# Kernel optimization log

Measured on AMD Instinct MI355X. Metric: run time of the kernel, lower is better.

The kernel has to match this reference:

```python
import jax, jax.numpy as jnp
import numpy as np

B, NE, NN, L = 64, 256, 1024, 512
F_IN, HID = 128, 128
VOCAB = 50000
ALPHA = 0.2
NEG = -9.0e15


def _leaky(z):
    return jnp.where(z >= 0, z, ALPHA * z)


def hga_layer(x, adj, W, W2, W3, a, a2, wc, transfer, concat):
    # x: [B, NN, Fin], adj: [B, NE, NN] (hyperedge incidence)
    O = W2.shape[1]
    x4 = x @ W2                      # [B, NN, O]
    if transfer:
        x = x @ W                    # [B, NN, O]
    # node->edge attention: score depends only on node k (query is shared word_context)
    s0 = wc[0] @ a[:O, 0]            # scalar
    e1 = _leaky(x4 @ a[O:, 0] + s0)  # [B, NN]
    e1 = jnp.broadcast_to(e1[:, None, :], adj.shape)          # [B, NE, NN]
    att_edge = jax.nn.softmax(jnp.where(adj > 0, e1, NEG), axis=2)
    edge = att_edge @ x              # [B, NE, O]
    edge4 = edge @ W3                # [B, NE, O]
    # edge->node attention: query = node feat x4[k], key = edge feat edge4[j]
    e2 = _leaky((x4 @ a2[:O, 0])[:, None, :] + (edge4 @ a2[O:, 0])[:, :, None])  # [B, NE, NN]
    att_node = jax.nn.softmax(jnp.where(adj > 0, e2, NEG).transpose(0, 2, 1), axis=2)  # [B, NN, NE]
    node = att_node @ edge           # [B, NN, O]
    return jax.nn.elu(node) if concat else node


def setup_inputs() -> dict:
    key = jax.random.key(0)
    ks = jax.random.split(key, 16)
    stdv = 1.0 / np.sqrt(HID)
    u = lambda k, shape: jax.random.uniform(k, shape, jnp.float32, -stdv, stdv)
    inp = {
        "items": jax.random.randint(ks[0], (B, NN), 0, VOCAB),
        "alias_inputs": jax.random.randint(ks[1], (B, L), 0, NN),
        "node_masks": jnp.ones((B, L), jnp.float32),
        "adj": jax.random.randint(ks[2], (B, NE, NN), 0, 2).astype(jnp.float32),
        "emb": jax.random.normal(ks[3], (VOCAB, F_IN), jnp.float32),
        # layer 1 (transfer=False, concat=True)
        "w2_1": u(ks[4], (F_IN, HID)),
        "w3_1": u(ks[5], (HID, HID)),
        "a_1": u(ks[6], (2 * HID, 1)),
        "a2_1": u(ks[7], (2 * HID, 1)),
        "wc_1": u(ks[8], (1, HID)),
        # layer 2 (transfer=True, concat=False)
        "w_2": u(ks[9], (HID, HID)),
        "w2_2": u(ks[10], (HID, HID)),
        "w3_2": u(ks[11], (HID, HID)),
        "a_2": u(ks[12], (2 * HID, 1)),
        "a2_2": u(ks[13], (2 * HID, 1)),
        "wc_2": u(ks[14], (1, HID)),
        "ln_g": jnp.ones((HID,), jnp.float32),
        "ln_b": jnp.zeros((HID,), jnp.float32),
    }
    return inp


def reference(items, alias_inputs, node_masks, adj, emb,
              w2_1, w3_1, a_1, a2_1, wc_1,
              w_2, w2_2, w3_2, a_2, a2_2, wc_2,
              ln_g, ln_b):
    hidden = emb[items]                                        # [B, NN, F]
    x = hga_layer(hidden, adj, None, w2_1, w3_1, a_1, a2_1, wc_1,
                  transfer=False, concat=True)
    x = hga_layer(x, adj, w_2, w2_2, w3_2, a_2, a2_2, wc_2,
                  transfer=True, concat=False)                 # [B, NN, HID]
    seq = jnp.take_along_axis(x, alias_inputs[:, :, None], axis=1)  # [B, L, HID]
    m = node_masks[:, :, None]
    h = seq * m
    b = jnp.sum(h * m, axis=-2) / jnp.sum(node_masks, -1, keepdims=True)  # [B, HID]
    mu = jnp.mean(b, -1, keepdims=True)
    var = jnp.mean((b - mu) ** 2, -1, keepdims=True)
    return (b - mu) / jnp.sqrt(var + 1e-6) * ln_g + ln_b
```

## Files before the change

### kernel.cpp

```cpp
#include <hip/hip_runtime.h>
#include <hip/hip_bf16.h>

typedef __hip_bfloat16 bf16;
typedef __attribute__((ext_vector_type(8))) unsigned short u16x8;
typedef __attribute__((ext_vector_type(4))) unsigned short u16x4;
typedef __attribute__((ext_vector_type(4))) float f32x4;
typedef __attribute__((ext_vector_type(8))) short bf16x8;

#define B_   64
#define NE_  256
#define NN_  1024
#define L_   512
#define HID_ 128
#define ALPHA_ 0.2f

__device__ __forceinline__ float bfu(unsigned short u){
  unsigned int x = ((unsigned int)u) << 16;
  union { unsigned int i; float f; } c; c.i = x; return c.f;
}
__device__ __forceinline__ unsigned short f2b(float f){
  bf16 h = __float2bfloat16(f);
  union { bf16 b; unsigned short u; } c; c.b = h; return c.u;
}
__device__ __forceinline__ int swz(int r, int c){ return (c ^ (r & 3) ^ ((r >> 2) & 3)) & 3; }

__global__ void k_small(const float* __restrict__ w2_1, const float* __restrict__ w3_1,
                        const float* __restrict__ a_1,  const float* __restrict__ a2_1,
                        const float* __restrict__ wc_1,
                        const float* __restrict__ w2_2, const float* __restrict__ w3_2,
                        const float* __restrict__ a_2,  const float* __restrict__ a2_2,
                        const float* __restrict__ wc_2,
                        const float* __restrict__ w_2,
                        const int* __restrict__ alias, const float* __restrict__ masks,
                        float* __restrict__ consts, unsigned short* __restrict__ W2T,
                        float* __restrict__ wcount, float* __restrict__ msum,
                        float* __restrict__ pooled)
{
  __shared__ float wcs[1024];
  __shared__ float red4[4];
  int blk = blockIdx.x, t = threadIdx.x;
  if (blk < 6) {
    if (t < 128) {
      const float* M; const float* v;
      switch (blk) {
        case 0: M = w2_1; v = a_1  + 128; break;
        case 1: M = w2_1; v = a2_1;       break;
        case 2: M = w3_1; v = a2_1 + 128; break;
        case 3: M = w2_2; v = a_2  + 128; break;
        case 4: M = w2_2; v = a2_2;       break;
        default: M = w3_2; v = a2_2 + 128; break;
      }
      float acc = 0.f;
      #pragma unroll 4
      for (int o = 0; o < 128; o += 4) {
        f32x4 m = *(const f32x4*)(M + t*128 + o);
        f32x4 x = *(const f32x4*)(v + o);
        acc += m[0]*x[0] + m[1]*x[1] + m[2]*x[2] + m[3]*x[3];
      }
      consts[blk*128 + t] = acc;
    }
  } else if (blk < 8) {
    const float* wc = (blk == 6) ? wc_1 : wc_2;
    const float* a  = (blk == 6) ? a_1  : a_2;
    if (t < 64) {
      float s = wc[t]*a[t] + wc[t+64]*a[t+64];
      #pragma unroll
      for (int sh = 32; sh > 0; sh >>= 1) s += __shfl_xor(s, sh);
      if (t == 0) consts[768 + (blk - 6)] = s;
    }
  } else if (blk == 8) {
    if (t < 128) for (int k = 0; k < 128; ++k) W2T[t*128 + k] = f2b(w_2[k*128 + t]);
  } else if (blk == 9) {
    for (int i = t; i < B_*HID_; i += 256) pooled[i] = 0.f;
  } else {
    int b = blk - 10;
    #pragma unroll
    for (int j = 0; j < 4; ++j) wcs[t + j*256] = 0.f;
    __syncthreads();
    float s = 0.f;
    #pragma unroll
    for (int j = 0; j < 2; ++j) {
      int l = t + j*256;
      float m = masks[b*L_ + l];
      int idx = alias[b*L_ + l];
      atomicAdd(&wcs[idx], m*m);
      s += m;
    }
    #pragma unroll
    for (int sh = 32; sh > 0; sh >>= 1) s += __shfl_xor(s, sh);
    if ((t & 63) == 0) red4[t >> 6] = s;
    __syncthreads();
    if (t == 0) msum[b] = red4[0] + red4[1] + red4[2] + red4[3];
    #pragma unroll
    for (int j = 0; j < 4; ++j) wcount[(long)b*NN_ + t + j*256] = wcs[t + j*256];
  }
}

__global__ __launch_bounds__(256) void k_prep(
    const float* __restrict__ adj,
    unsigned long long* __restrict__ ADJBb,
    unsigned short* __restrict__ ADJT16)
{
  __shared__ unsigned long long Lbits[16][17];
  const int id = blockIdx.x;
  const int b  = id & 63;
  const int ec = id >> 6;
  const int t  = threadIdx.x;
  const int wv = t >> 6, lane = t & 63;
  const int grp = lane >> 4;
  const int gl  = lane & 15;

  #pragma unroll
  for (int rr = 0; rr < 4; ++rr) {
    const int r = wv*4 + rr;
    const int e = ec*16 + r;
    const float* src = adj + ((long)b*NE_ + e)*NN_;
    #pragma unroll
    for (int i = 0; i < 4; ++i) {
      f32x4 v = *(const f32x4*)(src + i*256 + lane*4);
      unsigned long long nib =
            (unsigned long long)(v[0] != 0.f)
          | ((unsigned long long)(v[1] != 0.f) << 1)
          | ((unsigned long long)(v[2] != 0.f) << 2)
          | ((unsigned long long)(v[3] != 0.f) << 3);
      unsigned long long word = nib << (gl * 4);
      #pragma unroll
      for (int s = 1; s < 16; s <<= 1)
        word |= __shfl_xor(word, s);
      if (gl == 0) {
        Lbits[r][i*4 + grp] = word;
        ADJBb[((long)b*NE_ + e)*16 + i*4 + grp] = word;
      }
    }
  }
  __syncthreads();
  #pragma unroll
  for (int j = 0; j < 4; ++j) {
    int n = t + 256*j;
    int w = n >> 6, bitn = n & 63;
    unsigned int o = 0;
    #pragma unroll
    for (int rr = 0; rr < 16; ++rr)
      o |= (unsigned int)((Lbits[rr][w] >> bitn) & 1ull) << rr;
    ADJT16[((long)b*NN_ + n)*16 + ec] = (unsigned short)o;
  }
}

__global__ void k_fproj(const float* __restrict__ emb, const int* __restrict__ gitems,
                        const float* __restrict__ consts,
                        float* __restrict__ w1, float* __restrict__ f1,
                        unsigned short* __restrict__ YT)
{
  __shared__ float ce1s[128], cf1s[128];
  __shared__ __attribute__((aligned(16))) unsigned short T[64][132];
  int b = blockIdx.y, n0 = blockIdx.x * 64, t = threadIdx.x;
  if (t < 128) { ce1s[t] = consts[t]; cf1s[t] = consts[128 + t]; }
  __syncthreads();
  int r = t >> 2, h0 = (t & 3) * 32;
  long row = (long)b*NN_ + n0 + r;
  float s0 = consts[768];
  float xv[32];
  const float* sp = emb + (long)gitems[row]*HID_ + h0;
  #pragma unroll
  for (int j = 0; j < 32; j += 4) {
    f32x4 v = *(const f32x4*)(sp + j);
    #pragma unroll
    for (int k = 0; k < 4; ++k) xv[j+k] = v[k];
  }
  float p1 = 0.f, p2 = 0.f;
  #pragma unroll
  for (int j = 0; j < 32; ++j) { p1 += xv[j]*ce1s[h0+j]; p2 += xv[j]*cf1s[h0+j]; }
  p1 += __shfl_xor(p1, 1, 4); p1 += __shfl_xor(p1, 2, 4);
  p2 += __shfl_xor(p2, 1, 4); p2 += __shfl_xor(p2, 2, 4);
  float z = p1 + s0; z = (z >= 0.f) ? z : ALPHA_*z;
  float w = __expf(z);
  if ((t & 3) == 0) { w1[row] = w; f1[row] = p2; }
  #pragma unroll
  for (int j = 0; j < 32; j += 4) {
    u16x4 o;
    #pragma unroll
    for (int k = 0; k < 4; ++k) o[k] = f2b(w * xv[j+k]);
    *(u16x4*)&T[r][h0+j] = o;
  }
  __syncthreads();
  int h = t >> 1, nh = (t & 1) * 32;
  unsigned short* dst = YT + ((long)b*HID_ + h)*NN_ + n0 + nh;
  #pragma unroll
  for (int j = 0; j < 32; j += 8) {
    u16x8 o;
    #pragma unroll
    for (int k = 0; k < 8; ++k) o[k] = T[nh+j+k][h];
    *(u16x8*)&dst[j] = o;
  }
}

template<int TRANSFER>
__global__ __launch_bounds__(256) void k_gemm_edge(
    const unsigned char* __restrict__ ADJ8,
    const unsigned short* __restrict__ YT,
    const float* __restrict__ w1v,
    const float* __restrict__ consts, int layer,
    const unsigned short* __restrict__ W2T,
    unsigned short* __restrict__ ET,
    float* __restrict__ f2o)
{
  __shared__ __attribute__((aligned(16))) unsigned short SM[12288];
  __shared__ float dsum[64];
  const int id = blockIdx.x;
  const int b = id & 63;
  const long e0 = (long)(id >> 6) * 64;
  const int t = threadIdx.x;
  const int lane = t & 63;
  const int w = t >> 6, wm = w >> 1, wn = w & 1;
  const int r4 = t >> 2, c4 = t & 3;
  const int lr = lane & 15, g = lane >> 4;

  f32x4 acc[2][4];
  #pragma unroll
  for (int i = 0; i < 2; ++i)
    #pragma unroll
    for (int j = 0; j < 4; ++j) acc[i][j] = (f32x4){0.f,0.f,0.f,0.f};

  const unsigned char*  Ab = ADJ8 + ((long)b*NE_ + e0 + r4)*(NN_ >> 3);
  const unsigned short* Bb = YT + (long)b*HID_*NN_;
  const float*          wb = w1v + (long)b*NN_;

  unsigned int ab; u16x8 bv0, bv1; f32x4 wv0, wv1;
  float dot = 0.f;

  auto stage = [&](int kc) {
    ab  = Ab[(kc >> 3) + c4];
    wv0 = *(const f32x4*)(wb + kc + c4*8);
    wv1 = *(const f32x4*)(wb + kc + c4*8 + 4);
    bv0 = *(const u16x8*)(Bb + (long)r4*NN_ + kc + c4*8);
    bv1 = *(const u16x8*)(Bb + (long)(64+r4)*NN_ + kc + c4*8);
  };
  auto commit = [&](int buf) {
    u16x8 av;
    #pragma unroll
    for (int j = 0; j < 8; ++j) {
      unsigned int bit = (ab >> j) & 1u;
      av[j] = bit ? (unsigned short)0x3F80 : (unsigned short)0;
      float wj = (j < 4) ? wv0[j] : wv1[j-4];
      dot += bit ? wj : 0.f;
    }
    *(u16x8*)&SM[buf*2048 + r4*32 + swz(r4,c4)*8] = av;
    *(u16x8*)&SM[4096 + buf*4096 + r4*32 + swz(r4,c4)*8] = bv0;
    *(u16x8*)&SM[4096 + buf*4096 + (64+r4)*32 + swz(64+r4,c4)*8] = bv1;
  };

  stage(0); commit(0);
  int cur = 0;
  const int NIT = NN_/32;
  for (int it = 0; it < NIT; ++it) {
    __syncthreads();
    if (it+1 < NIT) stage((it+1)*32);
    const unsigned short* AsB = &SM[cur*2048];
    const unsigned short* BsB = &SM[4096 + cur*4096];
    bf16x8 af[2], bfr[4];
    #pragma unroll
    for (int mt = 0; mt < 2; ++mt) {
      int r = wm*32 + mt*16 + lr;
      af[mt] = *(const bf16x8*)&AsB[r*32 + swz(r,g)*8];
    }
    #pragma unroll
    for (int nt = 0; nt < 4; ++nt) {
      int n = wn*64 + nt*16 + lr;
      bfr[nt] = *(const bf16x8*)&BsB[n*32 + swz(n,g)*8];
    }
    #pragma unroll
    for (int mt = 0; mt < 2; ++mt)
      #pragma unroll
      for (int nt = 0; nt < 4; ++nt)
        acc[mt][nt] = __builtin_amdgcn_mfma_f32_16x16x32_bf16(af[mt], bfr[nt], acc[mt][nt], 0, 0, 0);
    if (it+1 < NIT) { commit(cur^1); cur ^= 1; }
  }
  dot += __shfl_down(dot, 2, 4); dot += __shfl_down(dot, 1, 4);
  if ((lane & 3) == 0) dsum[r4] = dot;
  __syncthreads();
  #pragma unroll
  for (int mt = 0; mt < 2; ++mt)
    #pragma unroll
    for (int nt = 0; nt < 4; ++nt) {
      int col = wn*64 + nt*16 + lr;
      #pragma unroll
      for (int q = 0; q < 4; ++q) {
        int rl = wm*32 + mt*16 + g*4 + q;
        SM[rl*136 + col] = f2b(acc[mt][nt][q] / dsum[rl]);
      }
    }
  __syncthreads();
  if (TRANSFER) {
    f32x4 acc2[2][4];
    #pragma unroll
    for (int i = 0; i < 2; ++i)
      #pragma unroll
      for (int j = 0; j < 4; ++j) acc2[i][j] = (f32x4){0.f,0.f,0.f,0.f};
    #pragma unroll
    for (int kc2 = 0; kc2 < 4; ++kc2) {
      bf16x8 af[2], bfr[4];
      #pragma unroll
      for (int mt = 0; mt < 2; ++mt) {
        int r = wm*32 + mt*16 + lr;
        af[mt] = *(const bf16x8*)&SM[r*136 + kc2*32 + g*8];
      }
      #pragma unroll
      for (int nt = 0; nt < 4; ++nt) {
        int n = wn*64 + nt*16 + lr;
        bfr[nt] = *(const bf16x8*)(W2T + n*128 + kc2*32 + g*8);
      }
      #pragma unroll
      for (int mt = 0; mt < 2; ++mt)
        #pragma unroll
        for (int nt = 0; nt < 4; ++nt)
          acc2[mt][nt] = __builtin_amdgcn_mfma_f32_16x16x32_bf16(af[mt], bfr[nt], acc2[mt][nt], 0, 0, 0);
    }
    __syncthreads();
    #pragma unroll
    for (int mt = 0; mt < 2; ++mt)
      #pragma unroll
      for (int nt = 0; nt < 4; ++nt) {
        int col = wn*64 + nt*16 + lr;
        #pragma unroll
        for (int q = 0; q < 4; ++q) {
          int rl = wm*32 + mt*16 + g*4 + q;
          SM[rl*136 + col] = f2b(acc2[mt][nt][q]);
        }
      }
    __syncthreads();
  }
  {
    const float* cf2 = consts + layer*384 + 256;
    int r = t >> 2, h0 = (t & 3) * 32;
    float p = 0.f;
    #pragma unroll
    for (int j = 0; j < 32; ++j) p += bfu(SM[r*136 + h0 + j]) * cf2[h0 + j];
    p += __shfl_down(p, 2, 4); p += __shfl_down(p, 1, 4);
    if ((t & 3) == 0) f2o[(long)b*NE_ + e0 + r] = p;
  }
  {
    int h = t >> 1, eh = (t & 1) * 32;
    unsigned short* dst = ET + ((long)b*HID_ + h)*NE_ + e0 + eh;
    #pragma unroll
    for (int j = 0; j < 32; j += 8) {
      u16x8 o;
      #pragma unroll
      for (int k = 0; k < 8; ++k) o[k] = SM[(eh+j+k)*136 + h];
      *(u16x8*)&dst[j] = o;
    }
  }
}

template<int EPI>
__global__ __launch_bounds__(256, 2) void k_gemm_att(
    const unsigned char* __restrict__ ADJ8,
    const unsigned short* __restrict__ ET,
    const float* __restrict__ f1v, const float* __restrict__ f2v,
    const float* __restrict__ consts,
    unsigned short* __restrict__ YTout, float* __restrict__ w1o, float* __restrict__ f1o,
    const float* __restrict__ wcount, float* __restrict__ pooled)
{
  __shared__ __attribute__((aligned(16))) unsigned short SM[12288];
  __shared__ float dsum[64];
  __shared__ float colsum[128];
  __shared__ float wrow[64];
  const int id = blockIdx.x;
  const int b = id & 63;
  const long m0 = (long)(id >> 6) * 64;
  const int t = threadIdx.x;
  const int lane = t & 63;
  const int w = t >> 6, wm = w >> 1, wn = w & 1;
  const int r4 = t >> 2, c4 = t & 3;
  const int lr = lane & 15, g = lane >> 4;

  f32x4 acc[2][4];
  #pragma unroll
  for (int i = 0; i < 2; ++i)
    #pragma unroll
    for (int j = 0; j < 4; ++j) acc[i][j] = (f32x4){0.f,0.f,0.f,0.f};

  const float f1r = f1v[(long)b*NN_ + m0 + r4];
  const unsigned char*  Ab = ADJ8 + ((long)b*NN_ + m0 + r4)*(NE_ >> 3);
  const unsigned short* Bb = ET + (long)b*HID_*NE_;
  const float* f2p = f2v + (long)b*NE_;

  unsigned int ab; u16x8 bv0, bv1; f32x4 fv0, fv1;
  float dot = 0.f;

  auto stage = [&](int kc) {
    ab  = Ab[(kc >> 3) + c4];
    fv0 = *(const f32x4*)(f2p + kc + c4*8);
    fv1 = *(const f32x4*)(f2p + kc + c4*8 + 4);
    bv0 = *(const u16x8*)(Bb + (long)r4*NE_ + kc + c4*8);
    bv1 = *(const u16x8*)(Bb + (long)(64+r4)*NE_ + kc + c4*8);
  };
  auto commit = [&](int buf) {
    u16x8 av;
    #pragma unroll
    for (int j = 0; j < 8; ++j) {
      unsigned int bit = (ab >> j) & 1u;
      float z = f1r + ((j < 4) ? fv0[j] : fv1[j-4]);
      z = (z >= 0.f) ? z : ALPHA_ * z;
      float wt = bit ? __expf(z) : 0.f;
      unsigned short us = f2b(wt);
      av[j] = us; dot += bfu(us);
    }
    *(u16x8*)&SM[buf*2048 + r4*32 + swz(r4,c4)*8] = av;
    *(u16x8*)&SM[4096 + buf*4096 + r4*32 + swz(r4,c4)*8] = bv0;
    *(u16x8*)&SM[4096 + buf*4096 + (64+r4)*32 + swz(64+r4,c4)*8] = bv1;
  };

  stage(0); commit(0);
  int cur = 0;
  const int NIT = NE_/32;
  for (int it = 0; it < NIT; ++it) {
    __syncthreads();
    if (it+1 < NIT) stage((it+1)*32);
    const unsigned short* AsB = &SM[cur*2048];
    const unsigned short* BsB = &SM[4096 + cur*4096];
    bf16x8 af[2], bfr[4];
    #pragma unroll
    for (int mt = 0; mt < 2; ++mt) {
      int r = wm*32 + mt*16 + lr;
      af[mt] = *(const bf16x8*)&AsB[r*32 + swz(r,g)*8];
    }
    #pragma unroll
    for (int nt = 0; nt < 4; ++nt) {
      int n = wn*64 + nt*16 + lr;
      bfr[nt] = *(const bf16x8*)&BsB[n*32 + swz(n,g)*8];
    }
    #pragma unroll
    for (int mt = 0; mt < 2; ++mt)
      #pragma unroll
      for (int nt = 0; nt < 4; ++nt)
        acc[mt][nt] = __builtin_amdgcn_mfma_f32_16x16x32_bf16(af[mt], bfr[nt], acc[mt][nt], 0, 0, 0);
    if (it+1 < NIT) { commit(cur^1); cur ^= 1; }
  }
  dot += __shfl_down(dot, 2, 4); dot += __shfl_down(dot, 1, 4);
  if ((lane & 3) == 0) dsum[r4] = dot;
  if (EPI == 2 && t < 128) colsum[t] = 0.f;
  __syncthreads();

  if (EPI == 1) {
    #pragma unroll
    for (int mt = 0; mt < 2; ++mt)
      #pragma unroll
      for (int nt = 0; nt < 4; ++nt) {
        int col = wn*64 + nt*16 + lr;
        #pragma unroll
        for (int q = 0; q < 4; ++q) {
          int rl = wm*32 + mt*16 + g*4 + q;
          float v = acc[mt][nt][q] / dsum[rl];
          v = (v > 0.f) ? v : expm1f(v);
          SM[rl*136 + col] = f2b(v);
        }
      }
    __syncthreads();
    {
      const float* ce1 = consts + 384;
      const float* cf1 = consts + 512;
      int r = t >> 2, h0 = (t & 3) * 32;
      float p1 = 0.f, p2 = 0.f;
      #pragma unroll
      for (int j = 0; j < 32; ++j) {
        float xv = bfu(SM[r*136 + h0 + j]);
        p1 += xv * ce1[h0 + j];
        p2 += xv * cf1[h0 + j];
      }
      p1 += __shfl_down(p1, 2, 4); p1 += __shfl_down(p1, 1, 4);
      p2 += __shfl_down(p2, 2, 4); p2 += __shfl_down(p2, 1, 4);
      if ((t & 3) == 0) {
        float z = p1 + consts[769];
        z = (z >= 0.f) ? z : ALPHA_ * z;
        float wv = __expf(z);
        wrow[r] = wv;
        w1o[(long)b*NN_ + m0 + r] = wv;
        f1o[(long)b*NN_ + m0 + r] = p2;
      }
    }
    __syncthreads();
    {
      int h = t >> 1, nh = (t & 1) * 32;
      unsigned short* dst = YTout + ((long)b*HID_ + h)*NN_ + m0 + nh;
      #pragma unroll
      for (int j = 0; j < 32; j += 8) {
        u16x8 o;
        #pragma unroll
        for (int k = 0; k < 8; ++k) {
          int rr = nh + j + k;
          o[k] = f2b(wrow[rr] * bfu(SM[rr*136 + h]));
        }
        *(u16x8*)&dst[j] = o;
      }
    }
  } else {
    float psum[4] = {0.f, 0.f, 0.f, 0.f};
    #pragma unroll
    for (int mt = 0; mt < 2; ++mt)
      #pragma unroll
      for (int q = 0; q < 4; ++q) {
        int rl = wm*32 + mt*16 + g*4 + q;
        float wc = wcount[(long)b*NN_ + m0 + rl];
        float inv = wc / dsum[rl];
        #pragma unroll
        for (int nt = 0; nt < 4; ++nt) psum[nt] += inv * acc[mt][nt][q];
      }
    #pragma unroll
    for (int nt = 0; nt < 4; ++nt) atomicAdd(&colsum[wn*64 + nt*16 + lr], psum[nt]);
    __syncthreads();
    if (t < 128) atomicAdd(&pooled[(long)b*HID_ + t], colsum[t]);
  }
}

__global__ void k_ln(const float* __restrict__ pooled, const float* __restrict__ msum,
                     const float* __restrict__ ln_g, const float* __restrict__ ln_b,
                     float* __restrict__ out)
{
  int b = blockIdx.x, t = threadIdx.x;
  __shared__ float sr[2];
  float bv = pooled[b*HID_ + t] / msum[b];
  int lane = t & 63;
  float p = bv;
  #pragma unroll
  for (int s = 32; s > 0; s >>= 1) p += __shfl_xor(p, s);
  if (lane == 0) sr[t >> 6] = p;
  __syncthreads();
  float mu = (sr[0] + sr[1]) * (1.f / HID_);
  float dv = bv - mu;
  p = dv * dv;
  #pragma unroll
  for (int s = 32; s > 0; s >>= 1) p += __shfl_xor(p, s);
  __syncthreads();
  if (lane == 0) sr[t >> 6] = p;
  __syncthreads();
  float var = (sr[0] + sr[1]) * (1.f / HID_);
  out[b*HID_ + t] = dv / sqrtf(var + 1e-6f) * ln_g[t] + ln_b[t];
}

extern "C" void kernel_launch(void* const* d_in, const int* in_sizes, int n_in,
                              void* d_out, int out_size, void* d_ws, size_t ws_size,
                              hipStream_t stream)
{
  const int*   items = (const int*)d_in[0];
  const int*   alias = (const int*)d_in[1];
  const float* masks = (const float*)d_in[2];
  const float* adj   = (const float*)d_in[3];
  const float* emb   = (const float*)d_in[4];
  const float* w2_1  = (const float*)d_in[5];
  const float* w3_1  = (const float*)d_in[6];
  const float* a_1   = (const float*)d_in[7];
  const float* a2_1  = (const float*)d_in[8];
  const float* wc_1  = (const float*)d_in[9];
  const float* w_2   = (const float*)d_in[10];
  const float* w2_2  = (const float*)d_in[11];
  const float* w3_2  = (const float*)d_in[12];
  const float* a_2   = (const float*)d_in[13];
  const float* a2_2  = (const float*)d_in[14];
  const float* wc_2  = (const float*)d_in[15];
  const float* ln_g  = (const float*)d_in[16];
  const float* ln_b  = (const float*)d_in[17];
  float* out = (float*)d_out;

  char* ws = (char*)d_ws;
  size_t off = 0;
  auto alloc = [&](size_t bytes) -> void* {
    void* p = ws + off; off += (bytes + 255) / 256 * 256; return p;
  };
  unsigned long long* ADJBb = (unsigned long long*)alloc((size_t)B_*NE_*(NN_/8));
  unsigned short*     ADJT16= (unsigned short*)    alloc((size_t)B_*NN_*(NE_/8));
  unsigned short* YT   = (unsigned short*)alloc((size_t)B_*HID_*NN_*2);
  unsigned short* ET   = (unsigned short*)alloc((size_t)B_*HID_*NE_*2);
  float* wcount= (float*)alloc((size_t)B_*NN_*4);
  float* pooled= (float*)alloc((size_t)B_*HID_*4);
  float* w1L1  = (float*)alloc((size_t)B_*NN_*4);
  float* f1L1  = (float*)alloc((size_t)B_*NN_*4);
  float* w1L2  = (float*)alloc((size_t)B_*NN_*4);
  float* f1L2  = (float*)alloc((size_t)B_*NN_*4);
  float* f2    = (float*)alloc((size_t)B_*NE_*4);
  float* msum  = (float*)alloc(B_*4);
  float* consts= (float*)alloc(772*4);
  unsigned short* W2T = (unsigned short*)alloc((size_t)HID_*HID_*2);
  if (off > ws_size) return;

  k_small<<<74, 256, 0, stream>>>(w2_1, w3_1, a_1, a2_1, wc_1, w2_2, w3_2, a_2, a2_2, wc_2,
                                  w_2, alias, masks, consts, W2T, wcount, msum, pooled);
  k_prep<<<B_*16, 256, 0, stream>>>(adj, ADJBb, ADJT16);
  k_fproj<<<dim3(NN_/64, B_), 256, 0, stream>>>(emb, items, consts, w1L1, f1L1, YT);

  k_gemm_edge<0><<<B_*(NE_/64), 256, 0, stream>>>((const unsigned char*)ADJBb, YT, w1L1,
        consts, 0, W2T, ET, f2);
  k_gemm_att<1><<<B_*(NN_/64), 256, 0, stream>>>((const unsigned char*)ADJT16, ET, f1L1, f2,
        consts, YT, w1L2, f1L2, nullptr, nullptr);

  k_gemm_edge<1><<<B_*(NE_/64), 256, 0, stream>>>((const unsigned char*)ADJBb, YT, w1L2,
        consts, 1, W2T, ET, f2);
  k_gemm_att<2><<<B_*(NN_/64), 256, 0, stream>>>((const unsigned char*)ADJT16, ET, f1L2, f2,
        consts, nullptr, nullptr, nullptr, wcount, pooled);

  k_ln<<<B_, HID_, 0, stream>>>(pooled, msum, ln_g, ln_b, out);
}
```

Measured before the change: 129.4 us.

## Retile edge GEMM to 32-row blocks and attention GEMM to 128-row blocks

```diff
diff --git a/kernel.cpp b/kernel.cpp
--- a/kernel.cpp
+++ b/kernel.cpp
@@ -195,7 +195,7 @@
 }
 
 template<int TRANSFER>
-__global__ __launch_bounds__(256) void k_gemm_edge(
+__global__ __launch_bounds__(256, 2) void k_gemm_edge(
     const unsigned char* __restrict__ ADJ8,
     const unsigned short* __restrict__ YT,
     const float* __restrict__ w1v,
@@ -204,49 +204,53 @@
     unsigned short* __restrict__ ET,
     float* __restrict__ f2o)
 {
-  __shared__ __attribute__((aligned(16))) unsigned short SM[12288];
-  __shared__ float dsum[64];
+  __shared__ __attribute__((aligned(16))) unsigned short SM[10240];
+  __shared__ float dsum[32];
   const int id = blockIdx.x;
   const int b = id & 63;
-  const long e0 = (long)(id >> 6) * 64;
+  const long e0 = (long)(id >> 6) * 32;
   const int t = threadIdx.x;
   const int lane = t & 63;
-  const int w = t >> 6, wm = w >> 1, wn = w & 1;
+  const int w = t >> 6;
   const int r4 = t >> 2, c4 = t & 3;
   const int lr = lane & 15, g = lane >> 4;
 
-  f32x4 acc[2][4];
+  f32x4 acc[2][2];
   #pragma unroll
   for (int i = 0; i < 2; ++i)
     #pragma unroll
-    for (int j = 0; j < 4; ++j) acc[i][j] = (f32x4){0.f,0.f,0.f,0.f};
-
-  const unsigned char*  Ab = ADJ8 + ((long)b*NE_ + e0 + r4)*(NN_ >> 3);
+    for (int j = 0; j < 2; ++j) acc[i][j] = (f32x4){0.f,0.f,0.f,0.f};
+
+  const unsigned char*  Ab = ADJ8 + ((long)b*NE_ + e0 + (t < 128 ? r4 : 0))*(NN_ >> 3);
   const unsigned short* Bb = YT + (long)b*HID_*NN_;
   const float*          wb = w1v + (long)b*NN_;
 
-  unsigned int ab; u16x8 bv0, bv1; f32x4 wv0, wv1;
+  unsigned int ab = 0; u16x8 bv0, bv1; f32x4 wv0, wv1;
   float dot = 0.f;
 
   auto stage = [&](int kc) {
-    ab  = Ab[(kc >> 3) + c4];
-    wv0 = *(const f32x4*)(wb + kc + c4*8);
-    wv1 = *(const f32x4*)(wb + kc + c4*8 + 4);
+    if (t < 128) {
+      ab  = Ab[(kc >> 3) + c4];
+      wv0 = *(const f32x4*)(wb + kc + c4*8);
+      wv1 = *(const f32x4*)(wb + kc + c4*8 + 4);
+    }
     bv0 = *(const u16x8*)(Bb + (long)r4*NN_ + kc + c4*8);
     bv1 = *(const u16x8*)(Bb + (long)(64+r4)*NN_ + kc + c4*8);
   };
   auto commit = [&](int buf) {
-    u16x8 av;
-    #pragma unroll
-    for (int j = 0; j < 8; ++j) {
-      unsigned int bit = (ab >> j) & 1u;
-      av[j] = bit ? (unsigned short)0x3F80 : (unsigned short)0;
-      float wj = (j < 4) ? wv0[j] : wv1[j-4];
-      dot += bit ? wj : 0.f;
-    }
-    *(u16x8*)&SM[buf*2048 + r4*32 + swz(r4,c4)*8] = av;
-    *(u16x8*)&SM[4096 + buf*4096 + r4*32 + swz(r4,c4)*8] = bv0;
-    *(u16x8*)&SM[4096 + buf*4096 + (64+r4)*32 + swz(64+r4,c4)*8] = bv1;
+    if (t < 128) {
+      u16x8 av;
+      #pragma unroll
+      for (int j = 0; j < 8; ++j) {
+        unsigned int bit = (ab >> j) & 1u;
+        av[j] = bit ? (unsigned short)0x3F80 : (unsigned short)0;
+        float wj = (j < 4) ? wv0[j] : wv1[j-4];
+        dot += bit ? wj : 0.f;
+      }
+      *(u16x8*)&SM[buf*1024 + r4*32 + swz(r4,c4)*8] = av;
+    }
+    *(u16x8*)&SM[2048 + buf*4096 + r4*32 + swz(r4,c4)*8] = bv0;
+    *(u16x8*)&SM[2048 + buf*4096 + (64+r4)*32 + swz(64+r4,c4)*8] = bv1;
   };
 
   stage(0); commit(0);
@@ -255,75 +259,77 @@
   for (int it = 0; it < NIT; ++it) {
     __syncthreads();
     if (it+1 < NIT) stage((it+1)*32);
-    const unsigned short* AsB = &SM[cur*2048];
-    const unsigned short* BsB = &SM[4096 + cur*4096];
-    bf16x8 af[2], bfr[4];
+    const unsigned short* AsB = &SM[cur*1024];
+    const unsigned short* BsB = &SM[2048 + cur*4096];
+    bf16x8 af[2], bfr[2];
     #pragma unroll
     for (int mt = 0; mt < 2; ++mt) {
-      int r = wm*32 + mt*16 + lr;
+      int r = mt*16 + lr;
       af[mt] = *(const bf16x8*)&AsB[r*32 + swz(r,g)*8];
     }
     #pragma unroll
-    for (int nt = 0; nt < 4; ++nt) {
-      int n = wn*64 + nt*16 + lr;
+    for (int nt = 0; nt < 2; ++nt) {
+      int n = w*32 + nt*16 + lr;
       bfr[nt] = *(const bf16x8*)&BsB[n*32 + swz(n,g)*8];
     }
     #pragma unroll
     for (int mt = 0; mt < 2; ++mt)
       #pragma unroll
-      for (int nt = 0; nt < 4; ++nt)
+      for (int nt = 0; nt < 2; ++nt)
         acc[mt][nt] = __builtin_amdgcn_mfma_f32_16x16x32_bf16(af[mt], bfr[nt], acc[mt][nt], 0, 0, 0);
     if (it+1 < NIT) { commit(cur^1); cur ^= 1; }
   }
-  dot += __shfl_down(dot, 2, 4); dot += __shfl_down(dot, 1, 4);
-  if ((lane & 3) == 0) dsum[r4] = dot;
+  if (t < 128) {
+    dot += __shfl_down(dot, 2, 4); dot += __shfl_down(dot, 1, 4);
+    if ((t & 3) == 0) dsum[r4] = dot;
+  }
   __syncthreads();
   #pragma unroll
   for (int mt = 0; mt < 2; ++mt)
     #pragma unroll
-    for (int nt = 0; nt < 4; ++nt) {
-      int col = wn*64 + nt*16 + lr;
+    for (int nt = 0; nt < 2; ++nt) {
+      int col = w*32 + nt*16 + lr;
       #pragma unroll
       for (int q = 0; q < 4; ++q) {
-        int rl = wm*32 + mt*16 + g*4 + q;
+        int rl = mt*16 + g*4 + q;
         SM[rl*136 + col] = f2b(acc[mt][nt][q] / dsum[rl]);
       }
     }
   __syncthreads();
   if (TRANSFER) {
-    f32x4 acc2[2][4];
+    f32x4 acc2[2][2];
     #pragma unroll
     for (int i = 0; i < 2; ++i)
       #pragma unroll
-      for (int j = 0; j < 4; ++j) acc2[i][j] = (f32x4){0.f,0.f,0.f,0.f};
+      for (int j = 0; j < 2; ++j) acc2[i][j] = (f32x4){0.f,0.f,0.f,0.f};
     #pragma unroll
     for (int kc2 = 0; kc2 < 4; ++kc2) {
-      bf16x8 af[2], bfr[4];
+      bf16x8 af[2], bfr[2];
       #pragma unroll
       for (int mt = 0; mt < 2; ++mt) {
-        int r = wm*32 + mt*16 + lr;
+        int r = mt*16 + lr;
         af[mt] = *(const bf16x8*)&SM[r*136 + kc2*32 + g*8];
       }
       #pragma unroll
-      for (int nt = 0; nt < 4; ++nt) {
-        int n = wn*64 + nt*16 + lr;
+      for (int nt = 0; nt < 2; ++nt) {
+        int n = w*32 + nt*16 + lr;
         bfr[nt] = *(const bf16x8*)(W2T + n*128 + kc2*32 + g*8);
       }
       #pragma unroll
       for (int mt = 0; mt < 2; ++mt)
         #pragma unroll
-        for (int nt = 0; nt < 4; ++nt)
+        for (int nt = 0; nt < 2; ++nt)
           acc2[mt][nt] = __builtin_amdgcn_mfma_f32_16x16x32_bf16(af[mt], bfr[nt], acc2[mt][nt], 0, 0, 0);
     }
     __syncthreads();
     #pragma unroll
     for (int mt = 0; mt < 2; ++mt)
       #pragma unroll
-      for (int nt = 0; nt < 4; ++nt) {
-        int col = wn*64 + nt*16 + lr;
+      for (int nt = 0; nt < 2; ++nt) {
+        int col = w*32 + nt*16 + lr;
         #pragma unroll
         for (int q = 0; q < 4; ++q) {
-          int rl = wm*32 + mt*16 + g*4 + q;
+          int rl = mt*16 + g*4 + q;
           SM[rl*136 + col] = f2b(acc2[mt][nt][q]);
         }
       }
@@ -331,18 +337,18 @@
   }
   {
     const float* cf2 = consts + layer*384 + 256;
-    int r = t >> 2, h0 = (t & 3) * 32;
+    int r = t >> 3, h0 = (t & 7) * 16;
     float p = 0.f;
     #pragma unroll
-    for (int j = 0; j < 32; ++j) p += bfu(SM[r*136 + h0 + j]) * cf2[h0 + j];
-    p += __shfl_down(p, 2, 4); p += __shfl_down(p, 1, 4);
-    if ((t & 3) == 0) f2o[(long)b*NE_ + e0 + r] = p;
+    for (int j = 0; j < 16; ++j) p += bfu(SM[r*136 + h0 + j]) * cf2[h0 + j];
+    p += __shfl_down(p, 4, 8); p += __shfl_down(p, 2, 8); p += __shfl_down(p, 1, 8);
+    if ((t & 7) == 0) f2o[(long)b*NE_ + e0 + r] = p;
   }
   {
-    int h = t >> 1, eh = (t & 1) * 32;
+    int h = t >> 1, eh = (t & 1) * 16;
     unsigned short* dst = ET + ((long)b*HID_ + h)*NE_ + e0 + eh;
     #pragma unroll
-    for (int j = 0; j < 32; j += 8) {
+    for (int j = 0; j < 16; j += 8) {
       u16x8 o;
       #pragma unroll
       for (int k = 0; k < 8; ++k) o[k] = SM[(eh+j+k)*136 + h];
@@ -360,54 +366,61 @@
     unsigned short* __restrict__ YTout, float* __restrict__ w1o, float* __restrict__ f1o,
     const float* __restrict__ wcount, float* __restrict__ pooled)
 {
-  __shared__ __attribute__((aligned(16))) unsigned short SM[12288];
-  __shared__ float dsum[64];
+  __shared__ __attribute__((aligned(16))) unsigned short SM[17408];
+  __shared__ float dsum[128];
   __shared__ float colsum[128];
-  __shared__ float wrow[64];
+  __shared__ float wrow[128];
   const int id = blockIdx.x;
   const int b = id & 63;
-  const long m0 = (long)(id >> 6) * 64;
+  const long m0 = (long)(id >> 6) * 128;
   const int t = threadIdx.x;
   const int lane = t & 63;
-  const int w = t >> 6, wm = w >> 1, wn = w & 1;
+  const int w = t >> 6;
   const int r4 = t >> 2, c4 = t & 3;
+  const int r2 = t >> 1, hf = t & 1;
   const int lr = lane & 15, g = lane >> 4;
 
-  f32x4 acc[2][4];
+  f32x4 acc[2][8];
   #pragma unroll
   for (int i = 0; i < 2; ++i)
     #pragma unroll
-    for (int j = 0; j < 4; ++j) acc[i][j] = (f32x4){0.f,0.f,0.f,0.f};
-
-  const float f1r = f1v[(long)b*NN_ + m0 + r4];
-  const unsigned char*  Ab = ADJ8 + ((long)b*NN_ + m0 + r4)*(NE_ >> 3);
+    for (int j = 0; j < 8; ++j) acc[i][j] = (f32x4){0.f,0.f,0.f,0.f};
+
+  const float f1r = f1v[(long)b*NN_ + m0 + r2];
+  const unsigned char*  Ab = ADJ8 + ((long)b*NN_ + m0 + r2)*(NE_ >> 3);
   const unsigned short* Bb = ET + (long)b*HID_*NE_;
   const float* f2p = f2v + (long)b*NE_;
 
-  unsigned int ab; u16x8 bv0, bv1; f32x4 fv0, fv1;
+  unsigned int ab; u16x8 bv0, bv1; f32x4 fv0, fv1, fv2, fv3;
   float dot = 0.f;
 
   auto stage = [&](int kc) {
-    ab  = Ab[(kc >> 3) + c4];
-    fv0 = *(const f32x4*)(f2p + kc + c4*8);
-    fv1 = *(const f32x4*)(f2p + kc + c4*8 + 4);
+    ab  = *(const unsigned short*)(Ab + (kc >> 3) + hf*2);
+    const float* fp = f2p + kc + hf*16;
+    fv0 = *(const f32x4*)(fp);
+    fv1 = *(const f32x4*)(fp + 4);
+    fv2 = *(const f32x4*)(fp + 8);
+    fv3 = *(const f32x4*)(fp + 12);
     bv0 = *(const u16x8*)(Bb + (long)r4*NE_ + kc + c4*8);
     bv1 = *(const u16x8*)(Bb + (long)(64+r4)*NE_ + kc + c4*8);
   };
   auto commit = [&](int buf) {
-    u16x8 av;
-    #pragma unroll
-    for (int j = 0; j < 8; ++j) {
+    u16x8 o0, o1;
+    #pragma unroll
+    for (int j = 0; j < 16; ++j) {
       unsigned int bit = (ab >> j) & 1u;
-      float z = f1r + ((j < 4) ? fv0[j] : fv1[j-4]);
+      float fz = (j < 4) ? fv0[j] : (j < 8) ? fv1[j-4] : (j < 12) ? fv2[j-8] : fv3[j-12];
+      float z = f1r + fz;
       z = (z >= 0.f) ? z : ALPHA_ * z;
       float wt = bit ? __expf(z) : 0.f;
       unsigned short us = f2b(wt);
-      av[j] = us; dot += bfu(us);
-    }
-    *(u16x8*)&SM[buf*2048 + r4*32 + swz(r4,c4)*8] = av;
-    *(u16x8*)&SM[4096 + buf*4096 + r4*32 + swz(r4,c4)*8] = bv0;
-    *(u16x8*)&SM[4096 + buf*4096 + (64+r4)*32 + swz(64+r4,c4)*8] = bv1;
+      if (j < 8) o0[j] = us; else o1[j-8] = us;
+      dot += bfu(us);
+    }
+    *(u16x8*)&SM[buf*4096 + r2*32 + swz(r2, hf*2)*8]   = o0;
+    *(u16x8*)&SM[buf*4096 + r2*32 + swz(r2, hf*2+1)*8] = o1;
+    *(u16x8*)&SM[8192 + buf*4096 + r4*32 + swz(r4,c4)*8] = bv0;
+    *(u16x8*)&SM[8192 + buf*4096 + (64+r4)*32 + swz(64+r4,c4)*8] = bv1;
   };
 
   stage(0); commit(0);
@@ -416,28 +429,28 @@
   for (int it = 0; it < NIT; ++it) {
     __syncthreads();
     if (it+1 < NIT) stage((it+1)*32);
-    const unsigned short* AsB = &SM[cur*2048];
-    const unsigned short* BsB = &SM[4096 + cur*4096];
-    bf16x8 af[2], bfr[4];
+    const unsigned short* AsB = &SM[cur*4096];
+    const unsigned short* BsB = &SM[8192 + cur*4096];
+    bf16x8 af[2], bfr[8];
     #pragma unroll
     for (int mt = 0; mt < 2; ++mt) {
-      int r = wm*32 + mt*16 + lr;
+      int r = w*32 + mt*16 + lr;
       af[mt] = *(const bf16x8*)&AsB[r*32 + swz(r,g)*8];
     }
     #pragma unroll
-    for (int nt = 0; nt < 4; ++nt) {
-      int n = wn*64 + nt*16 + lr;
+    for (int nt = 0; nt < 8; ++nt) {
+      int n = nt*16 + lr;
       bfr[nt] = *(const bf16x8*)&BsB[n*32 + swz(n,g)*8];
     }
     #pragma unroll
     for (int mt = 0; mt < 2; ++mt)
       #pragma unroll
-      for (int nt = 0; nt < 4; ++nt)
+      for (int nt = 0; nt < 8; ++nt)
         acc[mt][nt] = __builtin_amdgcn_mfma_f32_16x16x32_bf16(af[mt], bfr[nt], acc[mt][nt], 0, 0, 0);
     if (it+1 < NIT) { commit(cur^1); cur ^= 1; }
   }
-  dot += __shfl_down(dot, 2, 4); dot += __shfl_down(dot, 1, 4);
-  if ((lane & 3) == 0) dsum[r4] = dot;
+  dot += __shfl_down(dot, 1, 2);
+  if ((t & 1) == 0) dsum[r2] = dot;
   if (EPI == 2 && t < 128) colsum[t] = 0.f;
   __syncthreads();
 
@@ -445,11 +458,11 @@
     #pragma unroll
     for (int mt = 0; mt < 2; ++mt)
       #pragma unroll
-      for (int nt = 0; nt < 4; ++nt) {
-        int col = wn*64 + nt*16 + lr;
+      for (int nt = 0; nt < 8; ++nt) {
+        int col = nt*16 + lr;
         #pragma unroll
         for (int q = 0; q < 4; ++q) {
-          int rl = wm*32 + mt*16 + g*4 + q;
+          int rl = w*32 + mt*16 + g*4 + q;
           float v = acc[mt][nt][q] / dsum[rl];
           v = (v > 0.f) ? v : expm1f(v);
           SM[rl*136 + col] = f2b(v);
@@ -459,31 +472,31 @@
     {
       const float* ce1 = consts + 384;
       const float* cf1 = consts + 512;
-      int r = t >> 2, h0 = (t & 3) * 32;
+      int hh = hf * 64;
       float p1 = 0.f, p2 = 0.f;
       #pragma unroll
-      for (int j = 0; j < 32; ++j) {
-        float xv = bfu(SM[r*136 + h0 + j]);
-        p1 += xv * ce1[h0 + j];
-        p2 += xv * cf1[h0 + j];
-      }
-      p1 += __shfl_down(p1, 2, 4); p1 += __shfl_down(p1, 1, 4);
-      p2 += __shfl_down(p2, 2, 4); p2 += __shfl_down(p2, 1, 4);
-      if ((t & 3) == 0) {
+      for (int j = 0; j < 64; ++j) {
+        float xv = bfu(SM[r2*136 + hh + j]);
+        p1 += xv * ce1[hh + j];
+        p2 += xv * cf1[hh + j];
+      }
+      p1 += __shfl_down(p1, 1, 2);
+      p2 += __shfl_down(p2, 1, 2);
+      if ((t & 1) == 0) {
         float z = p1 + consts[769];
         z = (z >= 0.f) ? z : ALPHA_ * z;
         float wv = __expf(z);
-        wrow[r] = wv;
-        w1o[(long)b*NN_ + m0 + r] = wv;
-        f1o[(long)b*NN_ + m0 + r] = p2;
+        wrow[r2] = wv;
+        w1o[(long)b*NN_ + m0 + r2] = wv;
+        f1o[(long)b*NN_ + m0 + r2] = p2;
       }
     }
     __syncthreads();
     {
-      int h = t >> 1, nh = (t & 1) * 32;
+      int h = r2, nh = hf * 64;
       unsigned short* dst = YTout + ((long)b*HID_ + h)*NN_ + m0 + nh;
       #pragma unroll
-      for (int j = 0; j < 32; j += 8) {
+      for (int j = 0; j < 64; j += 8) {
         u16x8 o;
         #pragma unroll
         for (int k = 0; k < 8; ++k) {
@@ -494,19 +507,19 @@
       }
     }
   } else {
-    float psum[4] = {0.f, 0.f, 0.f, 0.f};
+    float psum[8] = {0.f,0.f,0.f,0.f,0.f,0.f,0.f,0.f};
     #pragma unroll
     for (int mt = 0; mt < 2; ++mt)
       #pragma unroll
       for (int q = 0; q < 4; ++q) {
-        int rl = wm*32 + mt*16 + g*4 + q;
+        int rl = w*32 + mt*16 + g*4 + q;
         float wc = wcount[(long)b*NN_ + m0 + rl];
         float inv = wc / dsum[rl];
         #pragma unroll
-        for (int nt = 0; nt < 4; ++nt) psum[nt] += inv * acc[mt][nt][q];
-      }
-    #pragma unroll
-    for (int nt = 0; nt < 4; ++nt) atomicAdd(&colsum[wn*64 + nt*16 + lr], psum[nt]);
+        for (int nt = 0; nt < 8; ++nt) psum[nt] += inv * acc[mt][nt][q];
+      }
+    #pragma unroll
+    for (int nt = 0; nt < 8; ++nt) atomicAdd(&colsum[nt*16 + lr], psum[nt]);
     __syncthreads();
     if (t < 128) atomicAdd(&pooled[(long)b*HID_ + t], colsum[t]);
   }
@@ -587,14 +600,14 @@
   k_prep<<<B_*16, 256, 0, stream>>>(adj, ADJBb, ADJT16);
   k_fproj<<<dim3(NN_/64, B_), 256, 0, stream>>>(emb, items, consts, w1L1, f1L1, YT);
 
-  k_gemm_edge<0><<<B_*(NE_/64), 256, 0, stream>>>((const unsigned char*)ADJBb, YT, w1L1,
+  k_gemm_edge<0><<<B_*(NE_/32), 256, 0, stream>>>((const unsigned char*)ADJBb, YT, w1L1,
         consts, 0, W2T, ET, f2);
-  k_gemm_att<1><<<B_*(NN_/64), 256, 0, stream>>>((const unsigned char*)ADJT16, ET, f1L1, f2,
+  k_gemm_att<1><<<B_*(NN_/128), 256, 0, stream>>>((const unsigned char*)ADJT16, ET, f1L1, f2,
         consts, YT, w1L2, f1L2, nullptr, nullptr);
 
-  k_gemm_edge<1><<<B_*(NE_/64), 256, 0, stream>>>((const unsigned char*)ADJBb, YT, w1L2,
+  k_gemm_edge<1><<<B_*(NE_/32), 256, 0, stream>>>((const unsigned char*)ADJBb, YT, w1L2,
         consts, 1, W2T, ET, f2);
-  k_gemm_att<2><<<B_*(NN_/64), 256, 0, stream>>>((const unsigned char*)ADJT16, ET, f1L2, f2,
+  k_gemm_att<2><<<B_*(NN_/128), 256, 0, stream>>>((const unsigned char*)ADJT16, ET, f1L2, f2,
         consts, nullptr, nullptr, nullptr, wcount, pooled);
 
   k_ln<<<B_, HID_, 0, stream>>>(pooled, msum, ln_g, ln_b, out);
```

After: 132.3 us. +2.2%, slower.
